# Kernel tuning notes

Hardware: AMD Instinct MI355X
Metric: run time of the kernel (lower is better)

## Reference

```python
import jax, jax.numpy as jnp
import numpy as np

EMB_DIM = 384
HEAD_DIM = 64
B, T = 512, 256


def setup_inputs() -> dict:
    key = jax.random.key(0)
    k1, k2, k3, k4 = jax.random.split(key, 4)
    inputs = jax.random.normal(k1, (B, T, EMB_DIM), dtype=jnp.float32)
    # torch nn.Linear weight layout: [out_features, in_features]
    s = EMB_DIM ** -0.5
    WQ = jax.random.normal(k2, (HEAD_DIM, EMB_DIM), dtype=jnp.float32) * s
    WK = jax.random.normal(k3, (HEAD_DIM, EMB_DIM), dtype=jnp.float32) * s
    WV = jax.random.normal(k4, (HEAD_DIM, EMB_DIM), dtype=jnp.float32) * s
    return {"inputs": inputs, "WQ": WQ, "WK": WK, "WV": WV}


def reference(inputs, WQ, WK, WV):
    # Linear (no bias): x @ W.T
    q = jnp.einsum('btc,dc->btd', inputs, WQ)  # [B,T,D]
    k = jnp.einsum('btc,dc->btd', inputs, WK)
    v = jnp.einsum('btc,dc->btd', inputs, WV)
    scale = k.shape[-1] ** -0.5
    scores = jnp.einsum('bqd,bkd->bqk', q, k) * scale  # [B,T,T]
    Tq = inputs.shape[1]
    causal = jnp.tril(jnp.ones((Tq, Tq), dtype=bool))
    scores = jnp.where(causal, scores, -jnp.inf)
    weights = jax.nn.softmax(scores, axis=-1)
    # dropout omitted (eval mode) for a deterministic reference
    out = jnp.einsum('bqk,bkd->bqd', weights, v)  # [B,T,D]
    return out
```

## Files before the change

### kernel.cpp

```cpp
#include <hip/hip_runtime.h>


typedef short s16x8 __attribute__((ext_vector_type(8)));
typedef float f32x4 __attribute__((ext_vector_type(4)));
typedef float f32x2 __attribute__((ext_vector_type(2)));
typedef unsigned int u32;
typedef unsigned int u32x4 __attribute__((ext_vector_type(4)));
typedef unsigned short u16;
typedef unsigned short u16x4 __attribute__((ext_vector_type(4)));
typedef __bf16 bf16x2 __attribute__((ext_vector_type(2)));

__device__ __forceinline__ u32 cvt2(float x, float y) {
  f32x2 v = {x, y};
  bf16x2 b = __builtin_convertvector(v, bf16x2);
  return __builtin_bit_cast(u32, b);
}
__device__ __forceinline__ u16 f2bf(float f) {
  __bf16 b = (__bf16)f;
  return __builtin_bit_cast(u16, b);
}
__device__ __forceinline__ s16x8 pack8(float4 a, float4 b) {
  u32x4 p = {cvt2(a.x, a.y), cvt2(a.z, a.w), cvt2(b.x, b.y), cvt2(b.z, b.w)};
  return __builtin_bit_cast(s16x8, p);
}

#define MFMA16 __builtin_amdgcn_mfma_f32_16x16x32_bf16

#define XC(b) ((b) * 16384)
#define WC(b) (32768 + (b) * 12288)
#define QS 57344
#define KS 90112
#define VS 122880

__global__ __launch_bounds__(1024) void head_kernel(
    const float* __restrict__ x,
    const float* __restrict__ WQ, const float* __restrict__ WK,
    const float* __restrict__ WV, float* __restrict__ out)
{
  __shared__ char smem[155648];
  const int tid = threadIdx.x;
  const int l  = tid & 63;
  const int w  = tid >> 6;
  const int g  = l >> 4, li = l & 15;
  const int wr = w >> 2, wc = w & 3;
  const long xbase = (long)blockIdx.x * (256 * 384);
  const long obase = (long)blockIdx.x * (256 * 64);

  const int srow  = tid >> 2;
  const int sslot = tid & 3;
  const bool do_w = (tid < 768);
  const float* wrp = nullptr;
  if (do_w)
    wrp = (srow < 64) ? (WQ + srow * 384)
         : (srow < 128) ? (WK + (srow - 64) * 384)
                        : (WV + (srow - 128) * 384);
  const int wswz = (srow >> 1) & 3;
  const int rswz = (li >> 1) & 3;

  {
    const float* px = x + xbase + srow * 384 + sslot * 8;
    float4 xa = *reinterpret_cast<const float4*>(px);
    float4 xb = *reinterpret_cast<const float4*>(px + 4);
    *reinterpret_cast<s16x8*>(smem + XC(0) + srow * 64 + ((sslot ^ wswz) << 4)) =
        pack8(xa, xb);
    if (do_w) {
      float4 wa = *reinterpret_cast<const float4*>(wrp + sslot * 8);
      float4 wb = *reinterpret_cast<const float4*>(wrp + sslot * 8 + 4);
      *reinterpret_cast<s16x8*>(smem + WC(0) + srow * 64 + ((sslot ^ wswz) << 4)) =
          pack8(wa, wb);
    }
  }
  __syncthreads();

  f32x4 acc[4][3];
#pragma unroll
  for (int bi = 0; bi < 4; ++bi)
#pragma unroll
    for (int ai = 0; ai < 3; ++ai)
      acc[bi][ai] = (f32x4){0.f, 0.f, 0.f, 0.f};

#pragma unroll 1
  for (int t = 0; t < 12; ++t) {
    float4 xa, xb, wa, wb;
    if (t < 11) {
      const float* px = x + xbase + srow * 384 + (t + 1) * 32 + sslot * 8;
      xa = *reinterpret_cast<const float4*>(px);
      xb = *reinterpret_cast<const float4*>(px + 4);
      if (do_w) {
        wa = *reinterpret_cast<const float4*>(wrp + (t + 1) * 32 + sslot * 8);
        wb = *reinterpret_cast<const float4*>(wrp + (t + 1) * 32 + sslot * 8 + 4);
      }
    }
    const int cb = t & 1;
    s16x8 bf[4];
#pragma unroll
    for (int bi = 0; bi < 4; ++bi)
      bf[bi] = *reinterpret_cast<const s16x8*>(
          smem + XC(cb) + (wr * 64 + bi * 16 + li) * 64 + ((g ^ rswz) << 4));
    s16x8 af[3];
#pragma unroll
    for (int ai = 0; ai < 3; ++ai)
      af[ai] = *reinterpret_cast<const s16x8*>(
          smem + WC(cb) + (wc * 48 + ai * 16 + li) * 64 + ((g ^ rswz) << 4));
#pragma unroll
    for (int bi = 0; bi < 4; ++bi)
#pragma unroll
      for (int ai = 0; ai < 3; ++ai)
        acc[bi][ai] = MFMA16(af[ai], bf[bi], acc[bi][ai], 0, 0, 0);

    if (t < 11) {
      *reinterpret_cast<s16x8*>(
          smem + XC(cb ^ 1) + srow * 64 + ((sslot ^ wswz) << 4)) = pack8(xa, xb);
      if (do_w)
        *reinterpret_cast<s16x8*>(
            smem + WC(cb ^ 1) + srow * 64 + ((sslot ^ wswz) << 4)) = pack8(wa, wb);
    }
    __syncthreads();
  }

#pragma unroll
  for (int bi = 0; bi < 4; ++bi) {
    const int row = wr * 64 + bi * 16 + li;
#pragma unroll
    for (int ai = 0; ai < 3; ++ai) {
      const int nb = wc * 48 + ai * 16;
      if (nb < 128) {
        const int b0 = (nb < 64) ? QS : KS;
        const int d16 = nb & 63;
        const int slot = (d16 >> 3) + (g >> 1);
        u16x4 pk;
        pk[0] = f2bf(acc[bi][ai][0]); pk[1] = f2bf(acc[bi][ai][1]);
        pk[2] = f2bf(acc[bi][ai][2]); pk[3] = f2bf(acc[bi][ai][3]);
        *reinterpret_cast<u16x4*>(
            smem + b0 + row * 128 + ((slot ^ (row & 7)) << 4) + (g & 1) * 8) = pk;
      } else {
#pragma unroll
        for (int r = 0; r < 4; ++r) {
          int d = nb - 128 + g * 4 + r;
          *reinterpret_cast<u16*>(
              smem + VS + d * 512 + ((row * 2) ^ ((d & 7) << 4))) =
              f2bf(acc[bi][ai][r]);
        }
      }
    }
  }
  __syncthreads();

  char* Pw = smem + w * 2048;
  const int qt = w;
  s16x8 qf[2];
#pragma unroll
  for (int dk = 0; dk < 2; ++dk) {
    int row = qt * 16 + li;
    qf[dk] = *reinterpret_cast<const s16x8*>(
        smem + QS + row * 128 + (((dk * 4 + g) ^ (row & 7)) << 4));
  }

  f32x4 o[4];
  float m[4], lsum[4];
#pragma unroll
  for (int r = 0; r < 4; ++r) { m[r] = -1e30f; lsum[r] = 0.f; }
#pragma unroll
  for (int nd = 0; nd < 4; ++nd) o[nd] = (f32x4){0.f, 0.f, 0.f, 0.f};

  const int nc = (qt >> 2) + 1;
#pragma unroll 1
  for (int c = 0; c < nc; ++c) {
    f32x4 s[4];
#pragma unroll
    for (int nj = 0; nj < 4; ++nj) s[nj] = (f32x4){0.f, 0.f, 0.f, 0.f};
#pragma unroll
    for (int dk = 0; dk < 2; ++dk) {
#pragma unroll
      for (int nj = 0; nj < 4; ++nj) {
        int rb = c * 64 + nj * 16 + li;
        s16x8 kf = *reinterpret_cast<const s16x8*>(
            smem + KS + rb * 128 + (((dk * 4 + g) ^ (rb & 7)) << 4));
        s[nj] = MFMA16(qf[dk], kf, s[nj], 0, 0, 0);
      }
    }
    const bool last = (c == nc - 1);
#pragma unroll
    for (int nj = 0; nj < 4; ++nj)
#pragma unroll
      for (int r = 0; r < 4; ++r) {
        float v = s[nj][r] * 0.125f;
        if (last && (c * 64 + nj * 16 + li) > (qt * 16 + g * 4 + r)) v = -1e30f;
        s[nj][r] = v;
      }
    float alpha[4];
#pragma unroll
    for (int r = 0; r < 4; ++r) {
      float pm = fmaxf(fmaxf(s[0][r], s[1][r]), fmaxf(s[2][r], s[3][r]));
      pm = fmaxf(pm, __shfl_xor(pm, 1));
      pm = fmaxf(pm, __shfl_xor(pm, 2));
      pm = fmaxf(pm, __shfl_xor(pm, 4));
      pm = fmaxf(pm, __shfl_xor(pm, 8));
      float mn = fmaxf(m[r], pm);
      alpha[r] = __expf(m[r] - mn);
      m[r] = mn;
    }
    float psum[4] = {0.f, 0.f, 0.f, 0.f};
#pragma unroll
    for (int nj = 0; nj < 4; ++nj)
#pragma unroll
      for (int r = 0; r < 4; ++r) {
        float p = __expf(s[nj][r] - m[r]);
        psum[r] += p;
        int rowp = g * 4 + r;
        *reinterpret_cast<u16*>(
            Pw + rowp * 128 + ((nj * 32 + li * 2) ^ ((rowp & 7) << 4))) = f2bf(p);
      }
#pragma unroll
    for (int r = 0; r < 4; ++r) {
      float ps = psum[r];
      ps += __shfl_xor(ps, 1);
      ps += __shfl_xor(ps, 2);
      ps += __shfl_xor(ps, 4);
      ps += __shfl_xor(ps, 8);
      lsum[r] = lsum[r] * alpha[r] + ps;
    }
#pragma unroll
    for (int nd = 0; nd < 4; ++nd)
#pragma unroll
      for (int r = 0; r < 4; ++r) o[nd][r] *= alpha[r];

    __asm__ volatile("s_waitcnt lgkmcnt(0)" ::: "memory");
    s16x8 pa[2];
#pragma unroll
    for (int kk = 0; kk < 2; ++kk)
      pa[kk] = *reinterpret_cast<const s16x8*>(
          Pw + li * 128 + (((kk * 4 + g) ^ (li & 7)) << 4));
#pragma unroll
    for (int nd = 0; nd < 4; ++nd) {
#pragma unroll
      for (int kk = 0; kk < 2; ++kk) {
        int d = nd * 16 + li;
        s16x8 vf = *reinterpret_cast<const s16x8*>(
            smem + VS + d * 512 + ((c * 128 + kk * 64 + g * 16) ^ ((d & 7) << 4)));
        o[nd] = MFMA16(pa[kk], vf, o[nd], 0, 0, 0);
      }
    }
  }
#pragma unroll
  for (int r = 0; r < 4; ++r) lsum[r] = 1.f / lsum[r];
#pragma unroll
  for (int nd = 0; nd < 4; ++nd)
#pragma unroll
    for (int r = 0; r < 4; ++r)
      out[obase + (qt * 16 + g * 4 + r) * 64 + nd * 16 + li] = o[nd][r] * lsum[r];
}

extern "C" void kernel_launch(void* const* d_in, const int* in_sizes, int n_in,
                              void* d_out, int out_size, void* d_ws, size_t ws_size,
                              hipStream_t stream) {
  const float* x  = (const float*)d_in[0];
  const float* WQ = (const float*)d_in[1];
  const float* WK = (const float*)d_in[2];
  const float* WV = (const float*)d_in[3];
  float* out = (float*)d_out;

  head_kernel<<<dim3(512), dim3(1024), 0, stream>>>(x, WQ, WK, WV, out);
}
```

Before: 62.01 us.

## Restructure fused head kernel to 512 threads with causal-balanced tiles and halved LDS

Shrinks the block from 1024 to 512 threads and the LDS footprint roughly by half, so more blocks can be resident per CU. Each wave now projects two 16-row query tiles (w and 15-w) to balance causal work. The x tile is converted straight from registers into MFMA operands instead of staging through LDS, and Q stays in registers. Attention uses 32-key chunks with a compact P buffer. The cost is extra barriers per K step and a second projection pass over the weights.

```diff
diff --git a/kernel.cpp b/kernel.cpp
--- a/kernel.cpp
+++ b/kernel.cpp
@@ -23,232 +23,259 @@
   u32x4 p = {cvt2(a.x, a.y), cvt2(a.z, a.w), cvt2(b.x, b.y), cvt2(b.z, b.w)};
   return __builtin_bit_cast(s16x8, p);
 }
+__device__ __forceinline__ s16x8 mk_qf(f32x4 a, f32x4 b) {
+  u32x4 p = {cvt2(a[0], a[1]), cvt2(a[2], a[3]), cvt2(b[0], b[1]), cvt2(b[2], b[3])};
+  return __builtin_bit_cast(s16x8, p);
+}
 
 #define MFMA16 __builtin_amdgcn_mfma_f32_16x16x32_bf16
 
-#define XC(b) ((b) * 16384)
-#define WC(b) (32768 + (b) * 12288)
-#define QS 57344
-#define KS 90112
-#define VS 122880
-
-__global__ __launch_bounds__(1024) void head_kernel(
+#define VTOF 32768
+#define WOFF 65536
+
+__device__ __forceinline__ void w_write(char* smem, int wrow, int wslot,
+                                        float4 a, float4 b) {
+  *reinterpret_cast<s16x8*>(smem + WOFF + wrow * 64 + ((wslot ^ (wrow & 3)) << 4)) =
+      pack8(a, b);
+}
+
+__device__ __forceinline__ void p1_compute(const char* smem, f32x4 (&acc)[12],
+                                           float4 x0, float4 x1, int g, int li) {
+  s16x8 xf = pack8(x0, x1);
+#pragma unroll
+  for (int h = 0; h < 3; ++h) {
+    s16x8 a0 = *reinterpret_cast<const s16x8*>(
+        smem + WOFF + ((h * 4 + 0) * 16 + li) * 64 + ((g ^ (li & 3)) << 4));
+    s16x8 a1 = *reinterpret_cast<const s16x8*>(
+        smem + WOFF + ((h * 4 + 1) * 16 + li) * 64 + ((g ^ (li & 3)) << 4));
+    s16x8 a2 = *reinterpret_cast<const s16x8*>(
+        smem + WOFF + ((h * 4 + 2) * 16 + li) * 64 + ((g ^ (li & 3)) << 4));
+    s16x8 a3 = *reinterpret_cast<const s16x8*>(
+        smem + WOFF + ((h * 4 + 3) * 16 + li) * 64 + ((g ^ (li & 3)) << 4));
+    acc[h * 4 + 0] = MFMA16(a0, xf, acc[h * 4 + 0], 0, 0, 0);
+    acc[h * 4 + 1] = MFMA16(a1, xf, acc[h * 4 + 1], 0, 0, 0);
+    acc[h * 4 + 2] = MFMA16(a2, xf, acc[h * 4 + 2], 0, 0, 0);
+    acc[h * 4 + 3] = MFMA16(a3, xf, acc[h * 4 + 3], 0, 0, 0);
+  }
+}
+
+__device__ __forceinline__ void p1_pass(
+    const float* __restrict__ xg, const float* __restrict__ wsrc1,
+    const float* __restrict__ wsrc2, char* __restrict__ smem,
+    f32x4 (&acc)[12], s16x8& qf0, s16x8& qf1,
+    const int tid, const int g, const int li, const int kvrow)
+{
+  const int wrow1 = tid >> 2, wslot = tid & 3, wrow2 = wrow1 + 128;
+  const bool dow2 = (tid < 256);
+
+  float4 ax0 = *reinterpret_cast<const float4*>(xg);
+  float4 ax1 = *reinterpret_cast<const float4*>(xg + 4);
+  float4 bx0, bx1;
+  float4 wa0, wa1, wb0, wb1;
+  wa0 = *reinterpret_cast<const float4*>(wsrc1);
+  wa1 = *reinterpret_cast<const float4*>(wsrc1 + 4);
+  if (dow2) {
+    wb0 = *reinterpret_cast<const float4*>(wsrc2);
+    wb1 = *reinterpret_cast<const float4*>(wsrc2 + 4);
+  }
+  w_write(smem, wrow1, wslot, wa0, wa1);
+  if (dow2) w_write(smem, wrow2, wslot, wb0, wb1);
+  __syncthreads();
+
+#pragma unroll 1
+  for (int it = 0; it < 6; ++it) {
+    const int t = it * 2;
+    if (t < 11) {
+      bx0 = *reinterpret_cast<const float4*>(xg + (t + 1) * 32);
+      bx1 = *reinterpret_cast<const float4*>(xg + (t + 1) * 32 + 4);
+      wa0 = *reinterpret_cast<const float4*>(wsrc1 + (t + 1) * 32);
+      wa1 = *reinterpret_cast<const float4*>(wsrc1 + (t + 1) * 32 + 4);
+      if (dow2) {
+        wb0 = *reinterpret_cast<const float4*>(wsrc2 + (t + 1) * 32);
+        wb1 = *reinterpret_cast<const float4*>(wsrc2 + (t + 1) * 32 + 4);
+      }
+    }
+    p1_compute(smem, acc, ax0, ax1, g, li);
+    __syncthreads();
+    if (t < 11) {
+      w_write(smem, wrow1, wslot, wa0, wa1);
+      if (dow2) w_write(smem, wrow2, wslot, wb0, wb1);
+    }
+    __syncthreads();
+
+    if (t + 2 < 12) {
+      ax0 = *reinterpret_cast<const float4*>(xg + (t + 2) * 32);
+      ax1 = *reinterpret_cast<const float4*>(xg + (t + 2) * 32 + 4);
+      wa0 = *reinterpret_cast<const float4*>(wsrc1 + (t + 2) * 32);
+      wa1 = *reinterpret_cast<const float4*>(wsrc1 + (t + 2) * 32 + 4);
+      if (dow2) {
+        wb0 = *reinterpret_cast<const float4*>(wsrc2 + (t + 2) * 32);
+        wb1 = *reinterpret_cast<const float4*>(wsrc2 + (t + 2) * 32 + 4);
+      }
+    }
+    p1_compute(smem, acc, bx0, bx1, g, li);
+    __syncthreads();
+    if (t + 2 < 12) {
+      w_write(smem, wrow1, wslot, wa0, wa1);
+      if (dow2) w_write(smem, wrow2, wslot, wb0, wb1);
+    }
+    __syncthreads();
+  }
+
+  qf0 = mk_qf(acc[0], acc[1]);
+  qf1 = mk_qf(acc[2], acc[3]);
+#pragma unroll
+  for (int mm = 0; mm < 4; ++mm) {
+    const int Eb = 32 * (mm >> 1) + 8 * g + 4 * (mm & 1);
+    u16x4 pk;
+    pk[0] = f2bf(acc[4 + mm][0]); pk[1] = f2bf(acc[4 + mm][1]);
+    pk[2] = f2bf(acc[4 + mm][2]); pk[3] = f2bf(acc[4 + mm][3]);
+    *reinterpret_cast<u16x4*>(smem + kvrow * 128 +
+        (((Eb >> 3) ^ (kvrow & 7)) << 4) + (Eb & 7) * 2) = pk;
+  }
+#pragma unroll
+  for (int mm = 0; mm < 4; ++mm)
+#pragma unroll
+    for (int r = 0; r < 4; ++r) {
+      const int d = mm * 16 + 4 * g + r;
+      *reinterpret_cast<u16*>(smem + VTOF + d * 512 +
+          ((kvrow * 2) ^ ((d & 7) << 4))) = f2bf(acc[8 + mm][r]);
+    }
+#pragma unroll
+  for (int nt = 0; nt < 12; ++nt) acc[nt] = (f32x4){0.f, 0.f, 0.f, 0.f};
+}
+
+__device__ __forceinline__ void attn_round(
+    char* __restrict__ smem, char* __restrict__ Pw,
+    float* __restrict__ outb, const int qt,
+    const s16x8 qf0, const s16x8 qf1, const int g, const int li)
+{
+  f32x4 o[4];
+  float mx[4], ls[4];
+#pragma unroll
+  for (int r = 0; r < 4; ++r) { mx[r] = -1e30f; ls[r] = 0.f; }
+#pragma unroll
+  for (int nd = 0; nd < 4; ++nd) o[nd] = (f32x4){0.f, 0.f, 0.f, 0.f};
+
+  const int nc = (qt >> 1) + 1;
+#pragma unroll 1
+  for (int c = 0; c < nc; ++c) {
+    f32x4 s0 = {0.f, 0.f, 0.f, 0.f}, s1 = {0.f, 0.f, 0.f, 0.f};
+    const int rb0 = c * 32 + li, rb1 = rb0 + 16;
+    s16x8 k00 = *reinterpret_cast<const s16x8*>(
+        smem + rb0 * 128 + (((g) ^ (rb0 & 7)) << 4));
+    s16x8 k01 = *reinterpret_cast<const s16x8*>(
+        smem + rb0 * 128 + (((4 + g) ^ (rb0 & 7)) << 4));
+    s16x8 k10 = *reinterpret_cast<const s16x8*>(
+        smem + rb1 * 128 + (((g) ^ (rb1 & 7)) << 4));
+    s16x8 k11 = *reinterpret_cast<const s16x8*>(
+        smem + rb1 * 128 + (((4 + g) ^ (rb1 & 7)) << 4));
+    s0 = MFMA16(qf0, k00, s0, 0, 0, 0);
+    s0 = MFMA16(qf1, k01, s0, 0, 0, 0);
+    s1 = MFMA16(qf0, k10, s1, 0, 0, 0);
+    s1 = MFMA16(qf1, k11, s1, 0, 0, 0);
+
+    const bool last = (c == nc - 1);
+    float alpha[4];
+#pragma unroll
+    for (int r = 0; r < 4; ++r) {
+      float v0 = s0[r] * 0.125f, v1 = s1[r] * 0.125f;
+      if (last) {
+        const int qrow = qt * 16 + 4 * g + r;
+        if (c * 32 + li > qrow) v0 = -1e30f;
+        if (c * 32 + 16 + li > qrow) v1 = -1e30f;
+      }
+      s0[r] = v0; s1[r] = v1;
+      float pm = fmaxf(v0, v1);
+      pm = fmaxf(pm, __shfl_xor(pm, 1));
+      pm = fmaxf(pm, __shfl_xor(pm, 2));
+      pm = fmaxf(pm, __shfl_xor(pm, 4));
+      pm = fmaxf(pm, __shfl_xor(pm, 8));
+      const float mn = fmaxf(mx[r], pm);
+      alpha[r] = __expf(mx[r] - mn);
+      mx[r] = mn;
+    }
+    float ps[4];
+#pragma unroll
+    for (int r = 0; r < 4; ++r) {
+      const float p0 = __expf(s0[r] - mx[r]);
+      const float p1 = __expf(s1[r] - mx[r]);
+      ps[r] = p0 + p1;
+      const int rp = 4 * g + r;
+      *reinterpret_cast<u16*>(Pw + rp * 80 + li * 2) = f2bf(p0);
+      *reinterpret_cast<u16*>(Pw + rp * 80 + 32 + li * 2) = f2bf(p1);
+    }
+#pragma unroll
+    for (int r = 0; r < 4; ++r) {
+      float t = ps[r];
+      t += __shfl_xor(t, 1);
+      t += __shfl_xor(t, 2);
+      t += __shfl_xor(t, 4);
+      t += __shfl_xor(t, 8);
+      ls[r] = ls[r] * alpha[r] + t;
+    }
+#pragma unroll
+    for (int nd = 0; nd < 4; ++nd)
+#pragma unroll
+      for (int r = 0; r < 4; ++r) o[nd][r] *= alpha[r];
+
+    __asm__ volatile("s_waitcnt lgkmcnt(0)" ::: "memory");
+    s16x8 pa = *reinterpret_cast<const s16x8*>(Pw + li * 80 + g * 16);
+#pragma unroll
+    for (int nd = 0; nd < 4; ++nd) {
+      const int d = nd * 16 + li;
+      s16x8 vf = *reinterpret_cast<const s16x8*>(
+          smem + VTOF + d * 512 + ((c * 64 + g * 16) ^ ((d & 7) << 4)));
+      o[nd] = MFMA16(pa, vf, o[nd], 0, 0, 0);
+    }
+  }
+#pragma unroll
+  for (int r = 0; r < 4; ++r) ls[r] = 1.f / ls[r];
+#pragma unroll
+  for (int nd = 0; nd < 4; ++nd)
+#pragma unroll
+    for (int r = 0; r < 4; ++r)
+      outb[(qt * 16 + 4 * g + r) * 64 + nd * 16 + li] = o[nd][r] * ls[r];
+}
+
+__global__ __launch_bounds__(512, 4) void head_kernel(
     const float* __restrict__ x,
     const float* __restrict__ WQ, const float* __restrict__ WK,
     const float* __restrict__ WV, float* __restrict__ out)
 {
-  __shared__ char smem[155648];
+  __shared__ char smem[77824];
   const int tid = threadIdx.x;
-  const int l  = tid & 63;
-  const int w  = tid >> 6;
-  const int g  = l >> 4, li = l & 15;
-  const int wr = w >> 2, wc = w & 3;
-  const long xbase = (long)blockIdx.x * (256 * 384);
-  const long obase = (long)blockIdx.x * (256 * 64);
-
-  const int srow  = tid >> 2;
-  const int sslot = tid & 3;
-  const bool do_w = (tid < 768);
-  const float* wrp = nullptr;
-  if (do_w)
-    wrp = (srow < 64) ? (WQ + srow * 384)
-         : (srow < 128) ? (WK + (srow - 64) * 384)
-                        : (WV + (srow - 128) * 384);
-  const int wswz = (srow >> 1) & 3;
-  const int rswz = (li >> 1) & 3;
+  const int l = tid & 63, w = tid >> 6;
+  const int g = l >> 4, li = l & 15;
+  const long bbase = (long)blockIdx.x * 256;
+
+  const int wrow1 = tid >> 2, wslot = tid & 3;
+  const float* wsrc1 = ((wrow1 < 64) ? (WQ + wrow1 * 384)
+                                     : (WK + (wrow1 - 64) * 384)) + wslot * 8;
+  const float* wsrc2 = WV + wrow1 * 384 + wslot * 8;
+
+  f32x4 acc[12];
+#pragma unroll
+  for (int nt = 0; nt < 12; ++nt) acc[nt] = (f32x4){0.f, 0.f, 0.f, 0.f};
+
+  s16x8 qfA0, qfA1, qfB0, qfB1;
 
   {
-    const float* px = x + xbase + srow * 384 + sslot * 8;
-    float4 xa = *reinterpret_cast<const float4*>(px);
-    float4 xb = *reinterpret_cast<const float4*>(px + 4);
-    *reinterpret_cast<s16x8*>(smem + XC(0) + srow * 64 + ((sslot ^ wswz) << 4)) =
-        pack8(xa, xb);
-    if (do_w) {
-      float4 wa = *reinterpret_cast<const float4*>(wrp + sslot * 8);
-      float4 wb = *reinterpret_cast<const float4*>(wrp + sslot * 8 + 4);
-      *reinterpret_cast<s16x8*>(smem + WC(0) + srow * 64 + ((sslot ^ wswz) << 4)) =
-          pack8(wa, wb);
-    }
+    const int rb = w * 16;
+    p1_pass(x + (bbase + rb + li) * 384 + g * 8, wsrc1, wsrc2, smem, acc,
+            qfA0, qfA1, tid, g, li, rb + li);
+  }
+  {
+    const int rb = (15 - w) * 16;
+    p1_pass(x + (bbase + rb + li) * 384 + g * 8, wsrc1, wsrc2, smem, acc,
+            qfB0, qfB1, tid, g, li, rb + li);
   }
   __syncthreads();
 
-  f32x4 acc[4][3];
-#pragma unroll
-  for (int bi = 0; bi < 4; ++bi)
-#pragma unroll
-    for (int ai = 0; ai < 3; ++ai)
-      acc[bi][ai] = (f32x4){0.f, 0.f, 0.f, 0.f};
-
-#pragma unroll 1
-  for (int t = 0; t < 12; ++t) {
-    float4 xa, xb, wa, wb;
-    if (t < 11) {
-      const float* px = x + xbase + srow * 384 + (t + 1) * 32 + sslot * 8;
-      xa = *reinterpret_cast<const float4*>(px);
-      xb = *reinterpret_cast<const float4*>(px + 4);
-      if (do_w) {
-        wa = *reinterpret_cast<const float4*>(wrp + (t + 1) * 32 + sslot * 8);
-        wb = *reinterpret_cast<const float4*>(wrp + (t + 1) * 32 + sslot * 8 + 4);
-      }
-    }
-    const int cb = t & 1;
-    s16x8 bf[4];
-#pragma unroll
-    for (int bi = 0; bi < 4; ++bi)
-      bf[bi] = *reinterpret_cast<const s16x8*>(
-          smem + XC(cb) + (wr * 64 + bi * 16 + li) * 64 + ((g ^ rswz) << 4));
-    s16x8 af[3];
-#pragma unroll
-    for (int ai = 0; ai < 3; ++ai)
-      af[ai] = *reinterpret_cast<const s16x8*>(
-          smem + WC(cb) + (wc * 48 + ai * 16 + li) * 64 + ((g ^ rswz) << 4));
-#pragma unroll
-    for (int bi = 0; bi < 4; ++bi)
-#pragma unroll
-      for (int ai = 0; ai < 3; ++ai)
-        acc[bi][ai] = MFMA16(af[ai], bf[bi], acc[bi][ai], 0, 0, 0);
-
-    if (t < 11) {
-      *reinterpret_cast<s16x8*>(
-          smem + XC(cb ^ 1) + srow * 64 + ((sslot ^ wswz) << 4)) = pack8(xa, xb);
-      if (do_w)
-        *reinterpret_cast<s16x8*>(
-            smem + WC(cb ^ 1) + srow * 64 + ((sslot ^ wswz) << 4)) = pack8(wa, wb);
-    }
-    __syncthreads();
-  }
-
-#pragma unroll
-  for (int bi = 0; bi < 4; ++bi) {
-    const int row = wr * 64 + bi * 16 + li;
-#pragma unroll
-    for (int ai = 0; ai < 3; ++ai) {
-      const int nb = wc * 48 + ai * 16;
-      if (nb < 128) {
-        const int b0 = (nb < 64) ? QS : KS;
-        const int d16 = nb & 63;
-        const int slot = (d16 >> 3) + (g >> 1);
-        u16x4 pk;
-        pk[0] = f2bf(acc[bi][ai][0]); pk[1] = f2bf(acc[bi][ai][1]);
-        pk[2] = f2bf(acc[bi][ai][2]); pk[3] = f2bf(acc[bi][ai][3]);
-        *reinterpret_cast<u16x4*>(
-            smem + b0 + row * 128 + ((slot ^ (row & 7)) << 4) + (g & 1) * 8) = pk;
-      } else {
-#pragma unroll
-        for (int r = 0; r < 4; ++r) {
-          int d = nb - 128 + g * 4 + r;
-          *reinterpret_cast<u16*>(
-              smem + VS + d * 512 + ((row * 2) ^ ((d & 7) << 4))) =
-              f2bf(acc[bi][ai][r]);
-        }
-      }
-    }
-  }
-  __syncthreads();
-
-  char* Pw = smem + w * 2048;
-  const int qt = w;
-  s16x8 qf[2];
-#pragma unroll
-  for (int dk = 0; dk < 2; ++dk) {
-    int row = qt * 16 + li;
-    qf[dk] = *reinterpret_cast<const s16x8*>(
-        smem + QS + row * 128 + (((dk * 4 + g) ^ (row & 7)) << 4));
-  }
-
-  f32x4 o[4];
-  float m[4], lsum[4];
-#pragma unroll
-  for (int r = 0; r < 4; ++r) { m[r] = -1e30f; lsum[r] = 0.f; }
-#pragma unroll
-  for (int nd = 0; nd < 4; ++nd) o[nd] = (f32x4){0.f, 0.f, 0.f, 0.f};
-
-  const int nc = (qt >> 2) + 1;
-#pragma unroll 1
-  for (int c = 0; c < nc; ++c) {
-    f32x4 s[4];
-#pragma unroll
-    for (int nj = 0; nj < 4; ++nj) s[nj] = (f32x4){0.f, 0.f, 0.f, 0.f};
-#pragma unroll
-    for (int dk = 0; dk < 2; ++dk) {
-#pragma unroll
-      for (int nj = 0; nj < 4; ++nj) {
-        int rb = c * 64 + nj * 16 + li;
-        s16x8 kf = *reinterpret_cast<const s16x8*>(
-            smem + KS + rb * 128 + (((dk * 4 + g) ^ (rb & 7)) << 4));
-        s[nj] = MFMA16(qf[dk], kf, s[nj], 0, 0, 0);
-      }
-    }
-    const bool last = (c == nc - 1);
-#pragma unroll
-    for (int nj = 0; nj < 4; ++nj)
-#pragma unroll
-      for (int r = 0; r < 4; ++r) {
-        float v = s[nj][r] * 0.125f;
-        if (last && (c * 64 + nj * 16 + li) > (qt * 16 + g * 4 + r)) v = -1e30f;
-        s[nj][r] = v;
-      }
-    float alpha[4];
-#pragma unroll
-    for (int r = 0; r < 4; ++r) {
-      float pm = fmaxf(fmaxf(s[0][r], s[1][r]), fmaxf(s[2][r], s[3][r]));
-      pm = fmaxf(pm, __shfl_xor(pm, 1));
-      pm = fmaxf(pm, __shfl_xor(pm, 2));
-      pm = fmaxf(pm, __shfl_xor(pm, 4));
-      pm = fmaxf(pm, __shfl_xor(pm, 8));
-      float mn = fmaxf(m[r], pm);
-      alpha[r] = __expf(m[r] - mn);
-      m[r] = mn;
-    }
-    float psum[4] = {0.f, 0.f, 0.f, 0.f};
-#pragma unroll
-    for (int nj = 0; nj < 4; ++nj)
-#pragma unroll
-      for (int r = 0; r < 4; ++r) {
-        float p = __expf(s[nj][r] - m[r]);
-        psum[r] += p;
-        int rowp = g * 4 + r;
-        *reinterpret_cast<u16*>(
-            Pw + rowp * 128 + ((nj * 32 + li * 2) ^ ((rowp & 7) << 4))) = f2bf(p);
-      }
-#pragma unroll
-    for (int r = 0; r < 4; ++r) {
-      float ps = psum[r];
-      ps += __shfl_xor(ps, 1);
-      ps += __shfl_xor(ps, 2);
-      ps += __shfl_xor(ps, 4);
-      ps += __shfl_xor(ps, 8);
-      lsum[r] = lsum[r] * alpha[r] + ps;
-    }
-#pragma unroll
-    for (int nd = 0; nd < 4; ++nd)
-#pragma unroll
-      for (int r = 0; r < 4; ++r) o[nd][r] *= alpha[r];
-
-    __asm__ volatile("s_waitcnt lgkmcnt(0)" ::: "memory");
-    s16x8 pa[2];
-#pragma unroll
-    for (int kk = 0; kk < 2; ++kk)
-      pa[kk] = *reinterpret_cast<const s16x8*>(
-          Pw + li * 128 + (((kk * 4 + g) ^ (li & 7)) << 4));
-#pragma unroll
-    for (int nd = 0; nd < 4; ++nd) {
-#pragma unroll
-      for (int kk = 0; kk < 2; ++kk) {
-        int d = nd * 16 + li;
-        s16x8 vf = *reinterpret_cast<const s16x8*>(
-            smem + VS + d * 512 + ((c * 128 + kk * 64 + g * 16) ^ ((d & 7) << 4)));
-        o[nd] = MFMA16(pa[kk], vf, o[nd], 0, 0, 0);
-      }
-    }
-  }
-#pragma unroll
-  for (int r = 0; r < 4; ++r) lsum[r] = 1.f / lsum[r];
-#pragma unroll
-  for (int nd = 0; nd < 4; ++nd)
-#pragma unroll
-    for (int r = 0; r < 4; ++r)
-      out[obase + (qt * 16 + g * 4 + r) * 64 + nd * 16 + li] = o[nd][r] * lsum[r];
+  char* Pw = smem + WOFF + w * 1536;
+  float* outb = out + bbase * 64;
+  attn_round(smem, Pw, outb, w, qfA0, qfA1, g, li);
+  attn_round(smem, Pw, outb, 15 - w, qfB0, qfB1, g, li);
 }
 
 extern "C" void kernel_launch(void* const* d_in, const int* in_sizes, int n_in,
@@ -260,5 +287,5 @@
   const float* WV = (const float*)d_in[3];
   float* out = (float*)d_out;
 
-  head_kernel<<<dim3(512), dim3(1024), 0, stream>>>(x, WQ, WK, WV, out);
-}
+  head_kernel<<<dim3(512), dim3(512), 0, stream>>>(x, WQ, WK, WV, out);
+}
```

Result: slower. 87.87 us (+41.7%).

## Stage full weights in LDS once and stream x directly into MFMA registers

Applied to the files above, without the earlier changes.

The projection stage now loads all three weight matrices into LDS (bf16, swizzled) once, and each wave reads its own 16 rows of x straight from global into register B-fragments with software prefetch. This removes the per-step x/W double-buffered LDS staging and its 12 block-wide barriers. Each wave computes the full 192-wide QKV for its rows, so Q stays in registers as MFMA fragments and only K and V^T are written to LDS. The cost is that every block re-reads the full weight set before starting, and each wave issues more LDS weight reads.

```diff
diff --git a/kernel.cpp b/kernel.cpp
--- a/kernel.cpp
+++ b/kernel.cpp
@@ -23,138 +23,106 @@
   u32x4 p = {cvt2(a.x, a.y), cvt2(a.z, a.w), cvt2(b.x, b.y), cvt2(b.z, b.w)};
   return __builtin_bit_cast(s16x8, p);
 }
+__device__ __forceinline__ s16x8 mk_qf(f32x4 a, f32x4 b) {
+  u32x4 p = {cvt2(a[0], a[1]), cvt2(a[2], a[3]), cvt2(b[0], b[1]), cvt2(b[2], b[3])};
+  return __builtin_bit_cast(s16x8, p);
+}
 
 #define MFMA16 __builtin_amdgcn_mfma_f32_16x16x32_bf16
 
-#define XC(b) ((b) * 16384)
-#define WC(b) (32768 + (b) * 12288)
-#define QS 57344
-#define KS 90112
-#define VS 122880
+#define VTOF 32768
+#define POFF 65536
 
 __global__ __launch_bounds__(1024) void head_kernel(
     const float* __restrict__ x,
     const float* __restrict__ WQ, const float* __restrict__ WK,
     const float* __restrict__ WV, float* __restrict__ out)
 {
-  __shared__ char smem[155648];
+  __shared__ char smem[147456];
   const int tid = threadIdx.x;
   const int l  = tid & 63;
   const int w  = tid >> 6;
   const int g  = l >> 4, li = l & 15;
-  const int wr = w >> 2, wc = w & 3;
-  const long xbase = (long)blockIdx.x * (256 * 384);
-  const long obase = (long)blockIdx.x * (256 * 64);
-
-  const int srow  = tid >> 2;
-  const int sslot = tid & 3;
-  const bool do_w = (tid < 768);
-  const float* wrp = nullptr;
-  if (do_w)
-    wrp = (srow < 64) ? (WQ + srow * 384)
-         : (srow < 128) ? (WK + (srow - 64) * 384)
-                        : (WV + (srow - 128) * 384);
-  const int wswz = (srow >> 1) & 3;
-  const int rswz = (li >> 1) & 3;
-
-  {
-    const float* px = x + xbase + srow * 384 + sslot * 8;
-    float4 xa = *reinterpret_cast<const float4*>(px);
-    float4 xb = *reinterpret_cast<const float4*>(px + 4);
-    *reinterpret_cast<s16x8*>(smem + XC(0) + srow * 64 + ((sslot ^ wswz) << 4)) =
-        pack8(xa, xb);
-    if (do_w) {
-      float4 wa = *reinterpret_cast<const float4*>(wrp + sslot * 8);
-      float4 wb = *reinterpret_cast<const float4*>(wrp + sslot * 8 + 4);
-      *reinterpret_cast<s16x8*>(smem + WC(0) + srow * 64 + ((sslot ^ wswz) << 4)) =
-          pack8(wa, wb);
-    }
+  const long bbase = (long)blockIdx.x * 256;
+
+  const int myrow = 16 * w + li;
+  const float* px = x + (bbase + myrow) * 384 + g * 8;
+
+  float4 a0 = *reinterpret_cast<const float4*>(px);
+  float4 a1 = *reinterpret_cast<const float4*>(px + 4);
+  float4 b0 = *reinterpret_cast<const float4*>(px + 32);
+  float4 b1 = *reinterpret_cast<const float4*>(px + 36);
+
+#pragma unroll 3
+  for (int i = 0; i < 9; ++i) {
+    int id = tid + 1024 * i;
+    int row = id / 48, slot = id - row * 48;
+    const float* wsrc = (row < 64) ? (WQ + row * 384)
+                       : (row < 128) ? (WK + (row - 64) * 384)
+                                     : (WV + (row - 128) * 384);
+    float4 wa = *reinterpret_cast<const float4*>(wsrc + slot * 8);
+    float4 wb = *reinterpret_cast<const float4*>(wsrc + slot * 8 + 4);
+    *reinterpret_cast<s16x8*>(smem + row * 768 + ((slot ^ (row & 7)) << 4)) =
+        pack8(wa, wb);
   }
   __syncthreads();
 
-  f32x4 acc[4][3];
-#pragma unroll
-  for (int bi = 0; bi < 4; ++bi)
-#pragma unroll
-    for (int ai = 0; ai < 3; ++ai)
-      acc[bi][ai] = (f32x4){0.f, 0.f, 0.f, 0.f};
+  f32x4 acc[12];
+#pragma unroll
+  for (int nt = 0; nt < 12; ++nt) acc[nt] = (f32x4){0.f, 0.f, 0.f, 0.f};
 
 #pragma unroll 1
-  for (int t = 0; t < 12; ++t) {
-    float4 xa, xb, wa, wb;
-    if (t < 11) {
-      const float* px = x + xbase + srow * 384 + (t + 1) * 32 + sslot * 8;
-      xa = *reinterpret_cast<const float4*>(px);
-      xb = *reinterpret_cast<const float4*>(px + 4);
-      if (do_w) {
-        wa = *reinterpret_cast<const float4*>(wrp + (t + 1) * 32 + sslot * 8);
-        wb = *reinterpret_cast<const float4*>(wrp + (t + 1) * 32 + sslot * 8 + 4);
-      }
-    }
-    const int cb = t & 1;
-    s16x8 bf[4];
-#pragma unroll
-    for (int bi = 0; bi < 4; ++bi)
-      bf[bi] = *reinterpret_cast<const s16x8*>(
-          smem + XC(cb) + (wr * 64 + bi * 16 + li) * 64 + ((g ^ rswz) << 4));
-    s16x8 af[3];
-#pragma unroll
-    for (int ai = 0; ai < 3; ++ai)
-      af[ai] = *reinterpret_cast<const s16x8*>(
-          smem + WC(cb) + (wc * 48 + ai * 16 + li) * 64 + ((g ^ rswz) << 4));
-#pragma unroll
-    for (int bi = 0; bi < 4; ++bi)
-#pragma unroll
-      for (int ai = 0; ai < 3; ++ai)
-        acc[bi][ai] = MFMA16(af[ai], bf[bi], acc[bi][ai], 0, 0, 0);
-
-    if (t < 11) {
-      *reinterpret_cast<s16x8*>(
-          smem + XC(cb ^ 1) + srow * 64 + ((sslot ^ wswz) << 4)) = pack8(xa, xb);
-      if (do_w)
-        *reinterpret_cast<s16x8*>(
-            smem + WC(cb ^ 1) + srow * 64 + ((sslot ^ wswz) << 4)) = pack8(wa, wb);
-    }
-    __syncthreads();
-  }
-
-#pragma unroll
-  for (int bi = 0; bi < 4; ++bi) {
-    const int row = wr * 64 + bi * 16 + li;
-#pragma unroll
-    for (int ai = 0; ai < 3; ++ai) {
-      const int nb = wc * 48 + ai * 16;
-      if (nb < 128) {
-        const int b0 = (nb < 64) ? QS : KS;
-        const int d16 = nb & 63;
-        const int slot = (d16 >> 3) + (g >> 1);
-        u16x4 pk;
-        pk[0] = f2bf(acc[bi][ai][0]); pk[1] = f2bf(acc[bi][ai][1]);
-        pk[2] = f2bf(acc[bi][ai][2]); pk[3] = f2bf(acc[bi][ai][3]);
-        *reinterpret_cast<u16x4*>(
-            smem + b0 + row * 128 + ((slot ^ (row & 7)) << 4) + (g & 1) * 8) = pk;
-      } else {
-#pragma unroll
-        for (int r = 0; r < 4; ++r) {
-          int d = nb - 128 + g * 4 + r;
-          *reinterpret_cast<u16*>(
-              smem + VS + d * 512 + ((row * 2) ^ ((d & 7) << 4))) =
-              f2bf(acc[bi][ai][r]);
-        }
-      }
+  for (int t = 0; t < 12; t += 2) {
+    s16x8 xfA = pack8(a0, a1);
+    if (t + 2 < 12) {
+      a0 = *reinterpret_cast<const float4*>(px + (t + 2) * 32);
+      a1 = *reinterpret_cast<const float4*>(px + (t + 2) * 32 + 4);
+    }
+#pragma unroll
+    for (int nt = 0; nt < 12; ++nt) {
+      const int rw = nt * 16 + li;
+      s16x8 af = *reinterpret_cast<const s16x8*>(
+          smem + rw * 768 + (((t * 4 + g) ^ (li & 7)) << 4));
+      acc[nt] = MFMA16(af, xfA, acc[nt], 0, 0, 0);
+    }
+    s16x8 xfB = pack8(b0, b1);
+    if (t + 3 < 12) {
+      b0 = *reinterpret_cast<const float4*>(px + (t + 3) * 32);
+      b1 = *reinterpret_cast<const float4*>(px + (t + 3) * 32 + 4);
+    }
+#pragma unroll
+    for (int nt = 0; nt < 12; ++nt) {
+      const int rw = nt * 16 + li;
+      s16x8 af = *reinterpret_cast<const s16x8*>(
+          smem + rw * 768 + ((((t + 1) * 4 + g) ^ (li & 7)) << 4));
+      acc[nt] = MFMA16(af, xfB, acc[nt], 0, 0, 0);
     }
   }
   __syncthreads();
 
-  char* Pw = smem + w * 2048;
+  s16x8 qf0 = mk_qf(acc[0], acc[1]);
+  s16x8 qf1 = mk_qf(acc[2], acc[3]);
+#pragma unroll
+  for (int mm = 0; mm < 4; ++mm) {
+    const int Eb = 32 * (mm >> 1) + 8 * g + 4 * (mm & 1);
+    u16x4 pk;
+    pk[0] = f2bf(acc[4 + mm][0]); pk[1] = f2bf(acc[4 + mm][1]);
+    pk[2] = f2bf(acc[4 + mm][2]); pk[3] = f2bf(acc[4 + mm][3]);
+    *reinterpret_cast<u16x4*>(smem + myrow * 128 +
+        (((Eb >> 3) ^ (myrow & 7)) << 4) + (Eb & 7) * 2) = pk;
+  }
+#pragma unroll
+  for (int mm = 0; mm < 4; ++mm)
+#pragma unroll
+    for (int r = 0; r < 4; ++r) {
+      const int d = mm * 16 + 4 * g + r;
+      *reinterpret_cast<u16*>(smem + VTOF + d * 512 +
+          ((myrow * 2) ^ ((d & 7) << 4))) = f2bf(acc[8 + mm][r]);
+    }
+  __syncthreads();
+
+  char* Pw = smem + POFF + w * 2048;
   const int qt = w;
-  s16x8 qf[2];
-#pragma unroll
-  for (int dk = 0; dk < 2; ++dk) {
-    int row = qt * 16 + li;
-    qf[dk] = *reinterpret_cast<const s16x8*>(
-        smem + QS + row * 128 + (((dk * 4 + g) ^ (row & 7)) << 4));
-  }
 
   f32x4 o[4];
   float m[4], lsum[4];
@@ -170,14 +138,14 @@
 #pragma unroll
     for (int nj = 0; nj < 4; ++nj) s[nj] = (f32x4){0.f, 0.f, 0.f, 0.f};
 #pragma unroll
-    for (int dk = 0; dk < 2; ++dk) {
-#pragma unroll
-      for (int nj = 0; nj < 4; ++nj) {
-        int rb = c * 64 + nj * 16 + li;
-        s16x8 kf = *reinterpret_cast<const s16x8*>(
-            smem + KS + rb * 128 + (((dk * 4 + g) ^ (rb & 7)) << 4));
-        s[nj] = MFMA16(qf[dk], kf, s[nj], 0, 0, 0);
-      }
+    for (int nj = 0; nj < 4; ++nj) {
+      const int rb = c * 64 + nj * 16 + li;
+      s16x8 kf0 = *reinterpret_cast<const s16x8*>(
+          smem + rb * 128 + (((0 + g) ^ (rb & 7)) << 4));
+      s16x8 kf1 = *reinterpret_cast<const s16x8*>(
+          smem + rb * 128 + (((4 + g) ^ (rb & 7)) << 4));
+      s[nj] = MFMA16(qf0, kf0, s[nj], 0, 0, 0);
+      s[nj] = MFMA16(qf1, kf1, s[nj], 0, 0, 0);
     }
     const bool last = (c == nc - 1);
 #pragma unroll
@@ -235,9 +203,9 @@
     for (int nd = 0; nd < 4; ++nd) {
 #pragma unroll
       for (int kk = 0; kk < 2; ++kk) {
-        int d = nd * 16 + li;
+        const int d = nd * 16 + li;
         s16x8 vf = *reinterpret_cast<const s16x8*>(
-            smem + VS + d * 512 + ((c * 128 + kk * 64 + g * 16) ^ ((d & 7) << 4)));
+            smem + VTOF + d * 512 + ((c * 128 + kk * 64 + g * 16) ^ ((d & 7) << 4)));
         o[nd] = MFMA16(pa[kk], vf, o[nd], 0, 0, 0);
       }
     }
@@ -248,7 +216,7 @@
   for (int nd = 0; nd < 4; ++nd)
 #pragma unroll
     for (int r = 0; r < 4; ++r)
-      out[obase + (qt * 16 + g * 4 + r) * 64 + nd * 16 + li] = o[nd][r] * lsum[r];
+      out[(bbase + qt * 16 + g * 4 + r) * 64 + nd * 16 + li] = o[nd][r] * lsum[r];
 }
 
 extern "C" void kernel_launch(void* const* d_in, const int* in_sizes, int n_in,
```

New measurement: 63.74 us. +2.8%, slower.
